# Kernel optimization log

Measured on AMD Instinct MI355X. Metric: run time of the kernel, lower is better.

The kernel has to match this reference:

```python
import jax, jax.numpy as jnp
import numpy as np


def _zoom(x, k, n):
    # x: [B, C, T, F]; zoom frequency axis by factor n/k via linear interpolation.
    # output[..., f] = w * x[..., floor(f*k/n)] + (1-w) * x[..., floor(f*k/n)+1]
    # where w = 1 - frac(f*k/n); out-of-range source indices contribute 0.
    if n == k:
        return x
    F_ = x.shape[3]
    f = jnp.arange(F_)
    pos = f * k                     # integer numerator of f*k/n
    idx = pos // n                  # floor(f*k/n)
    frac = (pos % n).astype(x.dtype) / jnp.asarray(n, x.dtype)
    w = 1.0 - frac                  # weight for lower neighbor, shape [F]
    if n == 1:
        # strided gather + zero pad (pure decimation, w == 1 everywhere)
        valid = idx < F_
        x0 = jnp.take(x, jnp.clip(idx, 0, F_ - 1), axis=3)
        return jnp.where(valid, x0, jnp.zeros((), x.dtype))
    valid0 = idx < F_
    valid1 = (idx + 1) < F_
    x0 = jnp.take(x, jnp.clip(idx, 0, F_ - 1), axis=3)
    x1 = jnp.take(x, jnp.clip(idx + 1, 0, F_ - 1), axis=3)
    out = jnp.where(valid0, w * x0, jnp.zeros((), x.dtype)) \
        + jnp.where(valid1, (1.0 - w) * x1, jnp.zeros((), x.dtype))
    return out


def setup_inputs() -> dict:
    key = jax.random.key(0)
    x = jax.random.normal(key, (8, 16, 256, 1024), dtype=jnp.float32)
    return {"input": x, "k": 2, "n": 3}


def reference(input, k, n):
    return _zoom(input, k, n)
```

## Files before the change

### kernel.cpp

```cpp
#include <hip/hip_runtime.h>


constexpr int F = 1024;
constexpr int VEC = 4;
constexpr int BLOCK = F / VEC;
constexpr int RU = 4;

__global__ __launch_bounds__(BLOCK) void zoom_kernel(
    const float* __restrict__ x,
    const int* __restrict__ kp,
    const int* __restrict__ np_,
    float* __restrict__ out,
    int nrows) {
  __shared__ float lds[RU][F];

  const int k = kp[0];
  const int n = np_[0];

  const int f0 = threadIdx.x * VEC;

  int  idx0[VEC], idx1[VEC];
  float w0[VEC], w1[VEC];
#pragma unroll
  for (int j = 0; j < VEC; ++j) {
    const int f   = f0 + j;
    const int pos = f * k;
    const int id  = pos / n;
    const int rem = pos - id * n;
    const float w = 1.0f - (float)rem / (float)n;
    const bool v0 = id < F;
    const bool v1 = (id + 1) < F;
    w0[j]   = v0 ? w : 0.0f;
    w1[j]   = v1 ? (1.0f - w) : 0.0f;
    idx0[j] = v0 ? id : 0;
    idx1[j] = v1 ? (id + 1) : (F - 1);
  }

  int nwords = ((F - 1) * k) / n + 2;
  if (nwords > F) nwords = F;

  const int nchunks = (nrows + RU - 1) / RU;

  for (int chunk = blockIdx.x; chunk < nchunks; chunk += gridDim.x) {
    const size_t row0 = (size_t)chunk * RU;
    const int rcnt = ((size_t)nrows - row0 < (size_t)RU) ? (int)(nrows - row0) : RU;

    for (int r = 0; r < rcnt; ++r) {
      const float* __restrict__ xr = x + (row0 + r) * F;
      for (int w = f0; w < nwords; w += BLOCK * VEC) {
        *reinterpret_cast<float4*>(&lds[r][w]) =
            *reinterpret_cast<const float4*>(xr + w);
      }
    }
    __syncthreads();

    for (int r = 0; r < rcnt; ++r) {
      float4 v;
      v.x = w0[0] * lds[r][idx0[0]] + w1[0] * lds[r][idx1[0]];
      v.y = w0[1] * lds[r][idx0[1]] + w1[1] * lds[r][idx1[1]];
      v.z = w0[2] * lds[r][idx0[2]] + w1[2] * lds[r][idx1[2]];
      v.w = w0[3] * lds[r][idx0[3]] + w1[3] * lds[r][idx1[3]];
      *reinterpret_cast<float4*>(out + (row0 + r) * F + f0) = v;
    }
    __syncthreads();
  }
}

extern "C" void kernel_launch(void* const* d_in, const int* in_sizes, int n_in,
                              void* d_out, int out_size, void* d_ws, size_t ws_size,
                              hipStream_t stream) {
  const float* x   = (const float*)d_in[0];
  const int*   kp  = (const int*)d_in[1];
  const int*   np_ = (const int*)d_in[2];
  float* out = (float*)d_out;

  const int total = in_sizes[0];
  const int nrows = total / F;

  const int nchunks = (nrows + RU - 1) / RU;
  const int grid = (nchunks < 2048) ? nchunks : 2048;
  zoom_kernel<<<grid, BLOCK, 0, stream>>>(x, kp, np_, out, nrows);
}
```

Before: 39.83 us.

## Double-buffer row staging with async global-to-LDS loads and nontemporal stores

The LDS tile is split into two buffers so the next chunk's input rows can be prefetched while the current chunk is interpolated. The prefetch uses the global_load_lds builtin, which writes global data straight into LDS without passing through registers, spread across the four waves in 256-float segments. Output writes become nontemporal stores, which hint that they should not stay in cache. The cost is twice the LDS per block, which may lower occupancy. The code also relies on __syncthreads to wait until the asynchronous loads have finished.

```diff
diff --git a/kernel.cpp b/kernel.cpp
--- a/kernel.cpp
+++ b/kernel.cpp
@@ -1,5 +1,7 @@
 #include <hip/hip_runtime.h>
 
+
+typedef float f32x4 __attribute__((ext_vector_type(4)));
 
 constexpr int F = 1024;
 constexpr int VEC = 4;
@@ -12,12 +14,14 @@
     const int* __restrict__ np_,
     float* __restrict__ out,
     int nrows) {
-  __shared__ float lds[RU][F];
+  __shared__ float lds[2][RU][F];
 
   const int k = kp[0];
   const int n = np_[0];
 
   const int f0 = threadIdx.x * VEC;
+  const int wv = threadIdx.x >> 6;
+  const int ln = threadIdx.x & 63;
 
   int  idx0[VEC], idx1[VEC];
   float w0[VEC], w1[VEC];
@@ -38,31 +42,49 @@
 
   int nwords = ((F - 1) * k) / n + 2;
   if (nwords > F) nwords = F;
+  const int segs = (nwords + 255) >> 8;
+  const int nstage = RU * segs;
 
   const int nchunks = (nrows + RU - 1) / RU;
 
-  for (int chunk = blockIdx.x; chunk < nchunks; chunk += gridDim.x) {
+  auto stage = [&](int chunk, int buf) {
     const size_t row0 = (size_t)chunk * RU;
-    const int rcnt = ((size_t)nrows - row0 < (size_t)RU) ? (int)(nrows - row0) : RU;
+    for (int s = wv; s < nstage; s += 4) {
+      const int r   = s / segs;
+      const int seg = s - r * segs;
+      size_t row = row0 + (size_t)r;
+      if (row >= (size_t)nrows) row = (size_t)nrows - 1;
+      const float* gp = x + row * F + seg * 256 + ln * 4;
+      float* lp = &lds[buf][r][seg * 256];
+      __builtin_amdgcn_global_load_lds(
+          (const __attribute__((address_space(1))) void*)gp,
+          (__attribute__((address_space(3))) void*)lp, 16, 0, 0);
+    }
+  };
 
-    for (int r = 0; r < rcnt; ++r) {
-      const float* __restrict__ xr = x + (row0 + r) * F;
-      for (int w = f0; w < nwords; w += BLOCK * VEC) {
-        *reinterpret_cast<float4*>(&lds[r][w]) =
-            *reinterpret_cast<const float4*>(xr + w);
-      }
+  const int c0 = blockIdx.x;
+  int cur = 0;
+  if (c0 < nchunks) stage(c0, 0);
+  __syncthreads();
+
+  for (int c = c0; c < nchunks; c += gridDim.x) {
+    const int cn = c + gridDim.x;
+    if (cn < nchunks) stage(cn, cur ^ 1);
+
+    const size_t row0 = (size_t)c * RU;
+#pragma unroll
+    for (int r = 0; r < RU; ++r) {
+      if (row0 + (size_t)r >= (size_t)nrows) break;
+      f32x4 v;
+      v.x = w0[0] * lds[cur][r][idx0[0]] + w1[0] * lds[cur][r][idx1[0]];
+      v.y = w0[1] * lds[cur][r][idx0[1]] + w1[1] * lds[cur][r][idx1[1]];
+      v.z = w0[2] * lds[cur][r][idx0[2]] + w1[2] * lds[cur][r][idx1[2]];
+      v.w = w0[3] * lds[cur][r][idx0[3]] + w1[3] * lds[cur][r][idx1[3]];
+      __builtin_nontemporal_store(v, (f32x4*)(out + (row0 + (size_t)r) * F + f0));
     }
+
     __syncthreads();
-
-    for (int r = 0; r < rcnt; ++r) {
-      float4 v;
-      v.x = w0[0] * lds[r][idx0[0]] + w1[0] * lds[r][idx1[0]];
-      v.y = w0[1] * lds[r][idx0[1]] + w1[1] * lds[r][idx1[1]];
-      v.z = w0[2] * lds[r][idx0[2]] + w1[2] * lds[r][idx1[2]];
-      v.w = w0[3] * lds[r][idx0[3]] + w1[3] * lds[r][idx1[3]];
-      *reinterpret_cast<float4*>(out + (row0 + r) * F + f0) = v;
-    }
-    __syncthreads();
+    cur ^= 1;
   }
 }
 
```

Measured after the change: 40.45 us. No clear change (+1.5%).
